# Kernel tuning notes

Measured on AMD Instinct MI355X. Metric: run time of the kernel, lower is better.

Reference implementation:

```python
import jax, jax.numpy as jnp
import numpy as np

D_MODEL = 1024
EXPAND = 2
D_INNER = D_MODEL * EXPAND  # 2048 independent SSM channels
D_STATE = 16
BATCH = 4
SEQ = 4096


def setup_inputs() -> dict:
    key = jax.random.key(0)
    ks = jax.random.split(key, 10)
    w = lambda k, shape, scale=0.02: jax.random.normal(k, shape, jnp.float32) * scale
    return {
        "x": jax.random.normal(ks[0], (BATCH, SEQ, D_MODEL), jnp.float32),
        "w_in": w(ks[1], (D_MODEL, D_INNER)),
        "b_in": jnp.zeros((D_INNER,), jnp.float32),
        "w_gate": w(ks[2], (D_MODEL, D_INNER)),
        "b_gate": jnp.zeros((D_INNER,), jnp.float32),
        # per-channel linear SSM params: h_t = A h_{t-1} + B x_t ; y_t = C . h_t
        "A": w(ks[3], (D_INNER, D_STATE, D_STATE), 0.05),  # small spectral radius -> stable recurrence
        "B_ssm": w(ks[4], (D_INNER, D_STATE), 0.1),
        "C_ssm": w(ks[5], (D_INNER, D_STATE), 0.1),
        "w_out": w(ks[6], (D_INNER, D_MODEL)),
        "b_out": jnp.zeros((D_MODEL,), jnp.float32),
    }


def reference(x, w_in, b_in, w_gate, b_gate, A, B_ssm, C_ssm, w_out, b_out):
    # x: [B, S, D]
    x_proj = x @ w_in + b_in                     # [B, S, C]
    gate = jax.nn.sigmoid(x @ w_gate + b_gate)   # [B, S, C]

    def step(h, xt):
        # h: [B, C, N] state for all channels; xt: [B, C] scalar input per channel
        h = jnp.einsum("cnm,bcm->bcn", A, h) + B_ssm[None] * xt[:, :, None]
        y = jnp.einsum("bcn,cn->bc", h, C_ssm)
        return h, y

    h0 = jnp.zeros((x.shape[0], D_INNER, D_STATE), x.dtype)
    xs = jnp.swapaxes(x_proj, 0, 1)              # [S, B, C]
    _, ys = jax.lax.scan(step, h0, xs)           # ys: [S, B, C]
    ssm_out = jnp.swapaxes(ys, 0, 1)             # [B, S, C]

    y = ssm_out * gate
    return y @ w_out + b_out                     # [B, S, D]
```

## Files before the change

kernel.cpp:

```cpp
#include <hip/hip_runtime.h>
#include <hip/hip_bf16.h>

#define D_MODEL 1024
#define D_INNER 2048
#define D_STATE 16
#define BATCH   4
#define SEQ     4096
#define MROWS   (BATCH * SEQ)

#define LTAPS 16
#define TSPAN 64

using bf16 = __hip_bfloat16;

typedef __attribute__((ext_vector_type(8))) short bf16x8;
typedef __attribute__((ext_vector_type(4))) float f32x4;

__device__ __forceinline__ float bf2f(bf16 v) { return __bfloat162float(v); }
__device__ __forceinline__ unsigned short f2bfbits(float f) {
  bf16 h = __float2bfloat16(f);
  return *(unsigned short*)&h;
}

#define AS1CAST(p) ((const __attribute__((address_space(1))) unsigned int*)(unsigned long long)(p))
#define AS3CAST(p) ((__attribute__((address_space(3))) unsigned int*)(unsigned long long)(p))

struct GemmCtx {
  const bf16* gptr[3];
  char*       lptr[3];
  int aoff[4], boff[4];
  int lane, wr, wc;
};

__device__ __forceinline__ void gemm_setup(
    GemmCtx& cx, const bf16* A, const bf16* BT, bf16* As, bf16* Bs,
    int m0, int n0, int K)
{
  const int tid  = threadIdx.x;
  cx.lane = tid & 63;
  const int wv = tid >> 6;
  cx.wr = wv >> 1;
  cx.wc = wv & 1;

  const int lrow = cx.lane >> 2;
  const int kch  = (((cx.lane & 3) ^ ((cx.lane >> 3) & 3)) * 8);
#pragma unroll
  for (int i = 0; i < 3; ++i) {
    const int s = wv * 3 + i;
    if (s < 16) {
      cx.gptr[i] = A + (size_t)(m0 + s * 16 + lrow) * K + kch;
      cx.lptr[i] = (char*)As + s * 1024;
    } else {
      const int t = s - 16;
      cx.gptr[i] = BT + (size_t)(n0 + t * 16 + lrow) * K + kch;
      cx.lptr[i] = (char*)Bs + t * 1024;
    }
  }
  const int fla = cx.lane & 15;
  const int cb  = cx.lane >> 4;
  const int csl = (cb ^ ((fla >> 1) & 3)) * 8;
#pragma unroll
  for (int i = 0; i < 4; ++i) {
    cx.aoff[i] = (cx.wr * 64 + i * 16 + fla) * 32 + csl;
    cx.boff[i] = (cx.wc * 64 + i * 16 + fla) * 32 + csl;
  }
}

__device__ __forceinline__ void gemm_kloop(
    GemmCtx& cx, const bf16* As, const bf16* Bs, f32x4 (&acc)[4][4], int K)
{
  for (int k0 = 0; k0 < K; k0 += 32) {
#pragma unroll
    for (int i = 0; i < 3; ++i)
      __builtin_amdgcn_global_load_lds(AS1CAST(cx.gptr[i]), AS3CAST(cx.lptr[i]), 16, 0, 0);
    cx.gptr[0] += 32; cx.gptr[1] += 32; cx.gptr[2] += 32;
    __syncthreads();

    bf16x8 af[4], bfr[4];
#pragma unroll
    for (int i = 0; i < 4; ++i) af[i]  = *(const bf16x8*)&As[cx.aoff[i]];
#pragma unroll
    for (int j = 0; j < 4; ++j) bfr[j] = *(const bf16x8*)&Bs[cx.boff[j]];

#pragma unroll
    for (int i = 0; i < 4; ++i)
#pragma unroll
      for (int j = 0; j < 4; ++j)
        acc[i][j] = __builtin_amdgcn_mfma_f32_16x16x32_bf16(af[i], bfr[j], acc[i][j], 0, 0, 0);
    __syncthreads();
  }
}

__global__ __launch_bounds__(512) void gemm_proj_dual(
    const bf16* __restrict__ A,
    const bf16* __restrict__ BT,
    const float* __restrict__ bias_in, const float* __restrict__ bias_gate,
    bf16* __restrict__ xp, bf16* __restrict__ gate)
{
  __shared__ alignas(16) bf16 As[256 * 32];
  __shared__ alignas(16) bf16 Bs[128 * 32];

  const int m0 = blockIdx.y * 256;
  const int n0 = blockIdx.x * 128;

  GemmCtx cx;
  gemm_setup(cx, A, BT, As, Bs, m0, n0, D_MODEL);

  f32x4 acc[4][4];
#pragma unroll
  for (int i = 0; i < 4; ++i)
#pragma unroll
    for (int j = 0; j < 4; ++j) acc[i][j] = (f32x4){0.f, 0.f, 0.f, 0.f};

  gemm_kloop(cx, As, Bs, acc, D_MODEL);

  const bool isGate = (n0 >= D_INNER);
  const int  nloc0  = n0 - (isGate ? D_INNER : 0);
  const float* bias = isGate ? bias_gate : bias_in;
  bf16* dst         = isGate ? gate : xp;

  const int crow = (cx.lane >> 4) * 4;
  const int ccol = cx.lane & 15;
#pragma unroll
  for (int i = 0; i < 4; ++i) {
#pragma unroll
    for (int j = 0; j < 4; ++j) {
      const int col = nloc0 + cx.wc * 64 + j * 16 + ccol;
      const float bcol = bias[col];
#pragma unroll
      for (int r = 0; r < 4; ++r) {
        const size_t row = (size_t)(m0 + cx.wr * 64 + i * 16 + crow + r);
        float v = acc[i][j][r] + bcol;
        if (isGate) v = 1.0f / (1.0f + __expf(-v));
        dst[row * D_INNER + col] = __float2bfloat16(v);
      }
    }
  }
}

__global__ __launch_bounds__(512) void gemm_out(
    const bf16* __restrict__ A,
    const bf16* __restrict__ BT,
    const float* __restrict__ bias,
    float* __restrict__ C)
{
  __shared__ alignas(16) bf16 As[256 * 32];
  __shared__ alignas(16) bf16 Bs[128 * 32];

  const int m0 = blockIdx.y * 256;
  const int n0 = blockIdx.x * 128;

  GemmCtx cx;
  gemm_setup(cx, A, BT, As, Bs, m0, n0, D_INNER);

  f32x4 acc[4][4];
#pragma unroll
  for (int i = 0; i < 4; ++i)
#pragma unroll
    for (int j = 0; j < 4; ++j) acc[i][j] = (f32x4){0.f, 0.f, 0.f, 0.f};

  gemm_kloop(cx, As, Bs, acc, D_INNER);

  const int crow = (cx.lane >> 4) * 4;
  const int ccol = cx.lane & 15;
#pragma unroll
  for (int i = 0; i < 4; ++i) {
#pragma unroll
    for (int j = 0; j < 4; ++j) {
      const int col = n0 + cx.wc * 64 + j * 16 + ccol;
      const float bcol = bias[col];
#pragma unroll
      for (int r = 0; r < 4; ++r) {
        const size_t row = (size_t)(m0 + cx.wr * 64 + i * 16 + crow + r);
        C[row * D_MODEL + col] = acc[i][j][r] + bcol;
      }
    }
  }
}

__global__ __launch_bounds__(256) void f32_to_bf16(
    const float* __restrict__ in, bf16* __restrict__ out, int n4)
{
  const int i = (blockIdx.x * 256 + threadIdx.x);
  if (i >= n4) return;
  const float4 v = *(const float4*)(in + (size_t)i * 4);
  ushort4 r;
  r.x = f2bfbits(v.x); r.y = f2bfbits(v.y); r.z = f2bfbits(v.z); r.w = f2bfbits(v.w);
  *(ushort4*)(out + (size_t)i * 4) = r;
}

__global__ __launch_bounds__(256) void transpose_to_bf16(
    const float* __restrict__ in, bf16* __restrict__ out, int R, int C)
{
  __shared__ float tile[32][33];
  const int c0 = blockIdx.x * 32, r0 = blockIdx.y * 32;
  const int tx = threadIdx.x & 31, ty = threadIdx.x >> 5;
#pragma unroll
  for (int i = ty; i < 32; i += 8)
    tile[i][tx] = in[(size_t)(r0 + i) * C + c0 + tx];
  __syncthreads();
#pragma unroll
  for (int i = ty; i < 32; i += 8)
    out[(size_t)(c0 + i) * R + r0 + tx] = __float2bfloat16(tile[tx][i]);
}

__device__ __forceinline__ float4 load4f(const float* p) { return *(const float4*)p; }

__global__ __launch_bounds__(256) void ssm_taps(
    const float* __restrict__ A, const float* __restrict__ Bv,
    const float* __restrict__ Cv, float* __restrict__ g)
{
  const int c = blockIdx.x * blockDim.x + threadIdx.x;
  if (c >= D_INNER) return;
  const float* Ac = A + (size_t)c * D_STATE * D_STATE;
  float v[D_STATE], cr[D_STATE];
#pragma unroll
  for (int i = 0; i < D_STATE; ++i) {
    v[i]  = Bv[(size_t)c * D_STATE + i];
    cr[i] = Cv[(size_t)c * D_STATE + i];
  }
  for (int m = 0; m < LTAPS; ++m) {
    float y = 0.f;
#pragma unroll
    for (int i = 0; i < D_STATE; ++i) y += cr[i] * v[i];
    g[(size_t)m * D_INNER + c] = y;
    float nv[D_STATE];
#pragma unroll
    for (int n = 0; n < D_STATE; ++n) {
      const float4 a0 = load4f(Ac + n * D_STATE + 0);
      const float4 a1 = load4f(Ac + n * D_STATE + 4);
      const float4 a2 = load4f(Ac + n * D_STATE + 8);
      const float4 a3 = load4f(Ac + n * D_STATE + 12);
      float s = a0.x * v[0] + a0.y * v[1] + a0.z * v[2] + a0.w * v[3];
      s += a1.x * v[4] + a1.y * v[5] + a1.z * v[6] + a1.w * v[7];
      s += a2.x * v[8] + a2.y * v[9] + a2.z * v[10] + a2.w * v[11];
      s += a3.x * v[12] + a3.y * v[13] + a3.z * v[14] + a3.w * v[15];
      nv[n] = s;
    }
#pragma unroll
    for (int i = 0; i < D_STATE; ++i) v[i] = nv[i];
  }
}

__global__ __launch_bounds__(256) void conv_gate(
    const bf16* __restrict__ xp, bf16* __restrict__ gate_io,
    const float* __restrict__ g)
{
  const int c  = blockIdx.x * blockDim.x + threadIdx.x;
  const int b  = blockIdx.z;
  const int t0 = blockIdx.y * TSPAN;

  float gg[LTAPS];
#pragma unroll
  for (int m = 0; m < LTAPS; ++m) gg[m] = g[(size_t)m * D_INNER + c];

  const size_t baseBC = ((size_t)b * SEQ) * D_INNER + c;

  float w[2 * LTAPS];
#pragma unroll
  for (int j = 0; j < LTAPS; ++j) {
    const int t = t0 - LTAPS + j;
    w[j] = (t >= 0) ? bf2f(xp[baseBC + (size_t)t * D_INNER]) : 0.f;
  }

  for (int blk = 0; blk < TSPAN; blk += LTAPS) {
#pragma unroll
    for (int j = 0; j < LTAPS; ++j)
      w[LTAPS + j] = bf2f(xp[baseBC + (size_t)(t0 + blk + j) * D_INNER]);
#pragma unroll
    for (int j = 0; j < LTAPS; ++j) {
      float y = 0.f;
#pragma unroll
      for (int m = 0; m < LTAPS; ++m) y += gg[m] * w[LTAPS + j - m];
      const size_t idx = baseBC + (size_t)(t0 + blk + j) * D_INNER;
      const float gt = bf2f(gate_io[idx]);
      gate_io[idx] = __float2bfloat16(y * gt);
    }
#pragma unroll
    for (int j = 0; j < LTAPS; ++j) w[j] = w[j + LTAPS];
  }
}

extern "C" void kernel_launch(void* const* d_in, const int* in_sizes, int n_in,
                              void* d_out, int out_size, void* d_ws, size_t ws_size,
                              hipStream_t stream)
{
  const float* x      = (const float*)d_in[0];
  const float* w_in   = (const float*)d_in[1];
  const float* b_in   = (const float*)d_in[2];
  const float* w_gate = (const float*)d_in[3];
  const float* b_gate = (const float*)d_in[4];
  const float* A      = (const float*)d_in[5];
  const float* B_ssm  = (const float*)d_in[6];
  const float* C_ssm  = (const float*)d_in[7];
  const float* w_out  = (const float*)d_in[8];
  const float* b_out  = (const float*)d_in[9];
  float* out = (float*)d_out;

  char* ws = (char*)d_ws;
  bf16*  gate  = (bf16*)(ws);
  bf16*  xbf   = (bf16*)(ws + 67108864);
  bf16*  wcatT = (bf16*)(ws + 100663296);
  bf16*  w_otT = (bf16*)(ws + 109051904);
  float* taps  = (float*)(ws + 113246208);
  bf16*  xp    = (bf16*)d_out;

  dim3 blk(256);

  hipLaunchKernelGGL(ssm_taps, dim3(D_INNER / 256), blk, 0, stream, A, B_ssm, C_ssm, taps);
  hipLaunchKernelGGL(f32_to_bf16, dim3((MROWS * D_MODEL / 4) / 256), blk, 0, stream,
                     x, xbf, MROWS * D_MODEL / 4);
  hipLaunchKernelGGL(transpose_to_bf16, dim3(D_INNER / 32, D_MODEL / 32), blk, 0, stream,
                     w_in, wcatT, D_MODEL, D_INNER);
  hipLaunchKernelGGL(transpose_to_bf16, dim3(D_INNER / 32, D_MODEL / 32), blk, 0, stream,
                     w_gate, wcatT + (size_t)D_INNER * D_MODEL, D_MODEL, D_INNER);
  hipLaunchKernelGGL(transpose_to_bf16, dim3(D_MODEL / 32, D_INNER / 32), blk, 0, stream,
                     w_out, w_otT, D_INNER, D_MODEL);

  dim3 gblk(512);
  dim3 g1(2 * D_INNER / 128, MROWS / 256);
  hipLaunchKernelGGL(gemm_proj_dual, g1, gblk, 0, stream,
                     xbf, wcatT, b_in, b_gate, xp, gate);

  dim3 gc(D_INNER / 256, SEQ / TSPAN, BATCH);
  hipLaunchKernelGGL(conv_gate, gc, blk, 0, stream, xp, gate, taps);

  dim3 g2(D_MODEL / 128, MROWS / 256);
  hipLaunchKernelGGL(gemm_out, g2, gblk, 0, stream, gate, w_otT, b_out, out);
}
```

Measured before the change: 461.4 us.

## Rewrite both GEMMs as 256x256 double-buffered pipelined kernels with block swizzle

Replaces the 256x128, K=32 single-buffered GEMM loop with a 256x256 tile, K=64 step and double-buffered LDS. Global-to-LDS loads for the next tiles are interleaved with four MFMA quadrants per step, using explicit vmcnt/lgkmcnt waits, barriers and s_setprio. Blocks are remapped through a swizzle to improve L2 reuse, and launch bounds request 2 blocks per CU. The goal is to hide memory latency and cut barrier stalls and redundant tile loads. In exchange it needs 128 KB of LDS per block and more registers, and the hand-written wait counts are fragile.

```diff
diff --git a/kernel.cpp b/kernel.cpp
--- a/kernel.cpp
+++ b/kernel.cpp
@@ -25,157 +25,256 @@
 #define AS1CAST(p) ((const __attribute__((address_space(1))) unsigned int*)(unsigned long long)(p))
 #define AS3CAST(p) ((__attribute__((address_space(3))) unsigned int*)(unsigned long long)(p))
 
-struct GemmCtx {
-  const bf16* gptr[3];
-  char*       lptr[3];
-  int aoff[4], boff[4];
-  int lane, wr, wc;
+#define FENCE() asm volatile("" ::: "memory")
+#define BAR() do { FENCE(); __builtin_amdgcn_s_barrier(); FENCE(); } while (0)
+#define WAIT_LGKM0() asm volatile("s_waitcnt lgkmcnt(0)" ::: "memory")
+
+#define TILE_E (256 * 64)
+
+struct G8 {
+  const bf16 *gA, *gB;
+  size_t K64, K128;
+  int stageLds;
+  int baseA0, baseA1;
+  int baseB0, baseB1;
+  int wr, wc, lane;
 };
 
-__device__ __forceinline__ void gemm_setup(
-    GemmCtx& cx, const bf16* A, const bf16* BT, bf16* As, bf16* Bs,
-    int m0, int n0, int K)
-{
-  const int tid  = threadIdx.x;
-  cx.lane = tid & 63;
+__device__ __forceinline__ void g8_setup(G8& g, const bf16* A, const bf16* BT,
+                                         int m0, int n0, int K)
+{
+  const int tid = threadIdx.x;
+  g.lane = tid & 63;
   const int wv = tid >> 6;
-  cx.wr = wv >> 1;
-  cx.wc = wv & 1;
-
-  const int lrow = cx.lane >> 2;
-  const int kch  = (((cx.lane & 3) ^ ((cx.lane >> 3) & 3)) * 8);
-#pragma unroll
-  for (int i = 0; i < 3; ++i) {
-    const int s = wv * 3 + i;
-    if (s < 16) {
-      cx.gptr[i] = A + (size_t)(m0 + s * 16 + lrow) * K + kch;
-      cx.lptr[i] = (char*)As + s * 1024;
-    } else {
-      const int t = s - 16;
-      cx.gptr[i] = BT + (size_t)(n0 + t * 16 + lrow) * K + kch;
-      cx.lptr[i] = (char*)Bs + t * 1024;
-    }
-  }
-  const int fla = cx.lane & 15;
-  const int cb  = cx.lane >> 4;
-  const int csl = (cb ^ ((fla >> 1) & 3)) * 8;
-#pragma unroll
-  for (int i = 0; i < 4; ++i) {
-    cx.aoff[i] = (cx.wr * 64 + i * 16 + fla) * 32 + csl;
-    cx.boff[i] = (cx.wc * 64 + i * 16 + fla) * 32 + csl;
-  }
-}
-
-__device__ __forceinline__ void gemm_kloop(
-    GemmCtx& cx, const bf16* As, const bf16* Bs, f32x4 (&acc)[4][4], int K)
-{
-  for (int k0 = 0; k0 < K; k0 += 32) {
-#pragma unroll
-    for (int i = 0; i < 3; ++i)
-      __builtin_amdgcn_global_load_lds(AS1CAST(cx.gptr[i]), AS3CAST(cx.lptr[i]), 16, 0, 0);
-    cx.gptr[0] += 32; cx.gptr[1] += 32; cx.gptr[2] += 32;
-    __syncthreads();
-
-    bf16x8 af[4], bfr[4];
-#pragma unroll
-    for (int i = 0; i < 4; ++i) af[i]  = *(const bf16x8*)&As[cx.aoff[i]];
-#pragma unroll
-    for (int j = 0; j < 4; ++j) bfr[j] = *(const bf16x8*)&Bs[cx.boff[j]];
-
-#pragma unroll
-    for (int i = 0; i < 4; ++i)
-#pragma unroll
-      for (int j = 0; j < 4; ++j)
-        acc[i][j] = __builtin_amdgcn_mfma_f32_16x16x32_bf16(af[i], bfr[j], acc[i][j], 0, 0, 0);
-    __syncthreads();
-  }
-}
-
-__global__ __launch_bounds__(512) void gemm_proj_dual(
+  g.wr = wv >> 2;
+  g.wc = wv & 3;
+  const int lr = g.lane >> 3, sl = g.lane & 7;
+  g.gA = A  + (size_t)(m0 + wv * 8 + lr) * K + (sl ^ lr) * 8;
+  g.gB = BT + (size_t)(n0 + wv * 8 + lr) * K + (sl ^ lr) * 8;
+  g.K64  = (size_t)64 * K;
+  g.K128 = (size_t)128 * K;
+  g.stageLds = wv * 8 * 64;
+  const int fla = g.lane & 15, cb = g.lane >> 4;
+  const int s0 = cb ^ (fla & 7), s1 = s0 ^ 4;
+  g.baseA0 = (g.wr * 64 + fla) * 64 + s0 * 8;
+  g.baseA1 = (g.wr * 64 + fla) * 64 + s1 * 8;
+  g.baseB0 = (g.wc * 32 + fla) * 64 + s0 * 8;
+  g.baseB1 = (g.wc * 32 + fla) * 64 + s1 * 8;
+}
+
+__device__ __forceinline__ void g8_stageA(const G8& g, bf16* dstTile, int h, int tau)
+{
+  const bf16* s = g.gA + (h ? g.K128 : (size_t)0) + (size_t)tau * 64;
+  bf16* d = dstTile + g.stageLds + h * (128 * 64);
+  __builtin_amdgcn_global_load_lds(AS1CAST(s), AS3CAST(d), 16, 0, 0);
+  __builtin_amdgcn_global_load_lds(AS1CAST(s + g.K64), AS3CAST(d + 64 * 64), 16, 0, 0);
+}
+
+__device__ __forceinline__ void g8_stageB(const G8& g, bf16* dstTile, int h, int tau)
+{
+  const bf16* s = g.gB + (h ? g.K128 : (size_t)0) + (size_t)tau * 64;
+  bf16* d = dstTile + g.stageLds + h * (128 * 64);
+  __builtin_amdgcn_global_load_lds(AS1CAST(s), AS3CAST(d), 16, 0, 0);
+  __builtin_amdgcn_global_load_lds(AS1CAST(s + g.K64), AS3CAST(d + 64 * 64), 16, 0, 0);
+}
+
+#define LOAD_A(MH) do { _Pragma("unroll") \
+  for (int mi = 0; mi < 4; ++mi) { \
+    af[mi][0] = *(const bf16x8*)&At[g.baseA0 + (MH) * 8192 + mi * 1024]; \
+    af[mi][1] = *(const bf16x8*)&At[g.baseA1 + (MH) * 8192 + mi * 1024]; \
+  } } while (0)
+
+#define LOAD_B(NH) do { _Pragma("unroll") \
+  for (int ni = 0; ni < 2; ++ni) { \
+    bfr[ni][0] = *(const bf16x8*)&Bt[g.baseB0 + (NH) * 8192 + ni * 1024]; \
+    bfr[ni][1] = *(const bf16x8*)&Bt[g.baseB1 + (NH) * 8192 + ni * 1024]; \
+  } } while (0)
+
+#define MFMA_Q(MH, NH) do { _Pragma("unroll") \
+  for (int mi = 0; mi < 4; ++mi) { _Pragma("unroll") \
+    for (int ni = 0; ni < 2; ++ni) { \
+      acc[MH][NH][mi][ni] = __builtin_amdgcn_mfma_f32_16x16x32_bf16( \
+          af[mi][0], bfr[ni][0], acc[MH][NH][mi][ni], 0, 0, 0); \
+      acc[MH][NH][mi][ni] = __builtin_amdgcn_mfma_f32_16x16x32_bf16( \
+          af[mi][1], bfr[ni][1], acc[MH][NH][mi][ni], 0, 0, 0); \
+    } } } while (0)
+
+__device__ __forceinline__ void g8_main(const G8& g, bf16* As, bf16* Bs,
+                                        f32x4 (&acc)[2][2][4][2], int K)
+{
+  const int nt = K >> 6;
+  bf16* A0 = As;  bf16* A1 = As + TILE_E;
+  bf16* B0 = Bs;  bf16* B1 = Bs + TILE_E;
+
+  g8_stageA(g, A0, 0, 0);
+  g8_stageB(g, B0, 1, 0);
+  g8_stageA(g, A0, 1, 0);
+  g8_stageB(g, B0, 0, 0);
+  if (nt > 1) {
+    g8_stageA(g, A1, 0, 1);
+    g8_stageB(g, B1, 1, 1);
+    g8_stageA(g, A1, 1, 1);
+    asm volatile("s_waitcnt vmcnt(6)" ::: "memory");
+  } else {
+    asm volatile("s_waitcnt vmcnt(0)" ::: "memory");
+  }
+  BAR();
+
+  bf16x8 af[4][2], bfr[2][2];
+
+  for (int t = 0; t < nt; ++t) {
+    const bf16* At = (t & 1) ? A1 : A0;
+    const bf16* Bt = (t & 1) ? B1 : B0;
+    bf16* Asame = (t & 1) ? A1 : A0;
+    bf16* Bsame = (t & 1) ? B1 : B0;
+    bf16* Bnext = (t & 1) ? B0 : B1;
+
+    LOAD_A(0); LOAD_B(0);
+    if (t + 1 < nt) g8_stageB(g, Bnext, 0, t + 1);
+    asm volatile("s_waitcnt lgkmcnt(8)" ::: "memory");
+    BAR();
+    WAIT_LGKM0();
+    __builtin_amdgcn_s_setprio(1);
+    MFMA_Q(0, 0);
+    __builtin_amdgcn_s_setprio(0);
+    BAR();
+
+    LOAD_B(1);
+    if (t + 2 < nt) g8_stageA(g, Asame, 0, t + 2);
+    BAR();
+    WAIT_LGKM0();
+    __builtin_amdgcn_s_setprio(1);
+    MFMA_Q(0, 1);
+    __builtin_amdgcn_s_setprio(0);
+    BAR();
+
+    LOAD_A(1);
+    if (t + 2 < nt) g8_stageB(g, Bsame, 1, t + 2);
+    BAR();
+    WAIT_LGKM0();
+    __builtin_amdgcn_s_setprio(1);
+    MFMA_Q(1, 1);
+    __builtin_amdgcn_s_setprio(0);
+    BAR();
+
+    LOAD_B(0);
+    if (t + 2 < nt) g8_stageA(g, Asame, 1, t + 2);
+    if (t < nt - 2) asm volatile("s_waitcnt vmcnt(6)" ::: "memory");
+    else            asm volatile("s_waitcnt vmcnt(0)" ::: "memory");
+    BAR();
+    WAIT_LGKM0();
+    __builtin_amdgcn_s_setprio(1);
+    MFMA_Q(1, 0);
+    __builtin_amdgcn_s_setprio(0);
+    BAR();
+  }
+}
+
+__global__ __launch_bounds__(512, 2) void gemm_proj_dual(
     const bf16* __restrict__ A,
     const bf16* __restrict__ BT,
     const float* __restrict__ bias_in, const float* __restrict__ bias_gate,
     bf16* __restrict__ xp, bf16* __restrict__ gate)
 {
-  __shared__ alignas(16) bf16 As[256 * 32];
-  __shared__ alignas(16) bf16 Bs[128 * 32];
-
-  const int m0 = blockIdx.y * 256;
-  const int n0 = blockIdx.x * 128;
-
-  GemmCtx cx;
-  gemm_setup(cx, A, BT, As, Bs, m0, n0, D_MODEL);
-
-  f32x4 acc[4][4];
-#pragma unroll
-  for (int i = 0; i < 4; ++i)
-#pragma unroll
-    for (int j = 0; j < 4; ++j) acc[i][j] = (f32x4){0.f, 0.f, 0.f, 0.f};
-
-  gemm_kloop(cx, As, Bs, acc, D_MODEL);
+  __shared__ alignas(16) bf16 As[2 * TILE_E];
+  __shared__ alignas(16) bf16 Bs[2 * TILE_E];
+
+  const int b = blockIdx.x;
+  const int swz = (b & 7) * 128 + (b >> 3);
+  const int bm = swz >> 4, bn = swz & 15;
+  const int m0 = bm * 256, n0 = bn * 256;
+
+  G8 g;
+  g8_setup(g, A, BT, m0, n0, D_MODEL);
+
+  f32x4 acc[2][2][4][2];
+#pragma unroll
+  for (int a1 = 0; a1 < 2; ++a1)
+#pragma unroll
+    for (int a2 = 0; a2 < 2; ++a2)
+#pragma unroll
+      for (int a3 = 0; a3 < 4; ++a3)
+#pragma unroll
+        for (int a4 = 0; a4 < 2; ++a4)
+          acc[a1][a2][a3][a4] = (f32x4){0.f, 0.f, 0.f, 0.f};
+
+  g8_main(g, As, Bs, acc, D_MODEL);
 
   const bool isGate = (n0 >= D_INNER);
   const int  nloc0  = n0 - (isGate ? D_INNER : 0);
   const float* bias = isGate ? bias_gate : bias_in;
   bf16* dst         = isGate ? gate : xp;
 
-  const int crow = (cx.lane >> 4) * 4;
-  const int ccol = cx.lane & 15;
-#pragma unroll
-  for (int i = 0; i < 4; ++i) {
-#pragma unroll
-    for (int j = 0; j < 4; ++j) {
-      const int col = nloc0 + cx.wc * 64 + j * 16 + ccol;
-      const float bcol = bias[col];
-#pragma unroll
-      for (int r = 0; r < 4; ++r) {
-        const size_t row = (size_t)(m0 + cx.wr * 64 + i * 16 + crow + r);
-        float v = acc[i][j][r] + bcol;
-        if (isGate) v = 1.0f / (1.0f + __expf(-v));
-        dst[row * D_INNER + col] = __float2bfloat16(v);
-      }
-    }
-  }
-}
-
-__global__ __launch_bounds__(512) void gemm_out(
+  const int crow = (g.lane >> 4) * 4;
+  const int ccol = g.lane & 15;
+#pragma unroll
+  for (int mh = 0; mh < 2; ++mh)
+#pragma unroll
+    for (int nh = 0; nh < 2; ++nh)
+#pragma unroll
+      for (int mi = 0; mi < 4; ++mi)
+#pragma unroll
+        for (int ni = 0; ni < 2; ++ni) {
+          const int col = nloc0 + nh * 128 + g.wc * 32 + ni * 16 + ccol;
+          const float bcol = bias[col];
+#pragma unroll
+          for (int r = 0; r < 4; ++r) {
+            const size_t row = (size_t)(m0 + mh * 128 + g.wr * 64 + mi * 16 + crow + r);
+            float v = acc[mh][nh][mi][ni][r] + bcol;
+            if (isGate) v = 1.0f / (1.0f + __expf(-v));
+            dst[row * D_INNER + col] = __float2bfloat16(v);
+          }
+        }
+}
+
+__global__ __launch_bounds__(512, 2) void gemm_out(
     const bf16* __restrict__ A,
     const bf16* __restrict__ BT,
     const float* __restrict__ bias,
     float* __restrict__ C)
 {
-  __shared__ alignas(16) bf16 As[256 * 32];
-  __shared__ alignas(16) bf16 Bs[128 * 32];
-
-  const int m0 = blockIdx.y * 256;
-  const int n0 = blockIdx.x * 128;
-
-  GemmCtx cx;
-  gemm_setup(cx, A, BT, As, Bs, m0, n0, D_INNER);
-
-  f32x4 acc[4][4];
-#pragma unroll
-  for (int i = 0; i < 4; ++i)
-#pragma unroll
-    for (int j = 0; j < 4; ++j) acc[i][j] = (f32x4){0.f, 0.f, 0.f, 0.f};
-
-  gemm_kloop(cx, As, Bs, acc, D_INNER);
-
-  const int crow = (cx.lane >> 4) * 4;
-  const int ccol = cx.lane & 15;
-#pragma unroll
-  for (int i = 0; i < 4; ++i) {
-#pragma unroll
-    for (int j = 0; j < 4; ++j) {
-      const int col = n0 + cx.wc * 64 + j * 16 + ccol;
-      const float bcol = bias[col];
-#pragma unroll
-      for (int r = 0; r < 4; ++r) {
-        const size_t row = (size_t)(m0 + cx.wr * 64 + i * 16 + crow + r);
-        C[row * D_MODEL + col] = acc[i][j][r] + bcol;
-      }
-    }
-  }
+  __shared__ alignas(16) bf16 As[2 * TILE_E];
+  __shared__ alignas(16) bf16 Bs[2 * TILE_E];
+
+  const int b = blockIdx.x;
+  const int swz = (b & 7) * 32 + (b >> 3);
+  const int bm = swz >> 2, bn = swz & 3;
+  const int m0 = bm * 256, n0 = bn * 256;
+
+  G8 g;
+  g8_setup(g, A, BT, m0, n0, D_INNER);
+
+  f32x4 acc[2][2][4][2];
+#pragma unroll
+  for (int a1 = 0; a1 < 2; ++a1)
+#pragma unroll
+    for (int a2 = 0; a2 < 2; ++a2)
+#pragma unroll
+      for (int a3 = 0; a3 < 4; ++a3)
+#pragma unroll
+        for (int a4 = 0; a4 < 2; ++a4)
+          acc[a1][a2][a3][a4] = (f32x4){0.f, 0.f, 0.f, 0.f};
+
+  g8_main(g, As, Bs, acc, D_INNER);
+
+  const int crow = (g.lane >> 4) * 4;
+  const int ccol = g.lane & 15;
+#pragma unroll
+  for (int mh = 0; mh < 2; ++mh)
+#pragma unroll
+    for (int nh = 0; nh < 2; ++nh)
+#pragma unroll
+      for (int mi = 0; mi < 4; ++mi)
+#pragma unroll
+        for (int ni = 0; ni < 2; ++ni) {
+          const int col = n0 + nh * 128 + g.wc * 32 + ni * 16 + ccol;
+          const float bcol = bias[col];
+#pragma unroll
+          for (int r = 0; r < 4; ++r) {
+            const size_t row = (size_t)(m0 + mh * 128 + g.wr * 64 + mi * 16 + crow + r);
+            C[row * D_MODEL + col] = acc[mh][nh][mi][ni][r] + bcol;
+          }
+        }
 }
 
 __global__ __launch_bounds__(256) void f32_to_bf16(
@@ -318,13 +417,12 @@
                      w_out, w_otT, D_INNER, D_MODEL);
 
   dim3 gblk(512);
-  dim3 g1(2 * D_INNER / 128, MROWS / 256);
-  hipLaunchKernelGGL(gemm_proj_dual, g1, gblk, 0, stream,
+  hipLaunchKernelGGL(gemm_proj_dual, dim3((2 * D_INNER / 256) * (MROWS / 256)), gblk, 0, stream,
                      xbf, wcatT, b_in, b_gate, xp, gate);
 
   dim3 gc(D_INNER / 256, SEQ / TSPAN, BATCH);
   hipLaunchKernelGGL(conv_gate, gc, blk, 0, stream, xp, gate, taps);
 
-  dim3 g2(D_MODEL / 128, MROWS / 256);
-  hipLaunchKernelGGL(gemm_out, g2, gblk, 0, stream, gate, w_otT, b_out, out);
-}
+  hipLaunchKernelGGL(gemm_out, dim3((D_MODEL / 256) * (MROWS / 256)), gblk, 0, stream,
+                     gate, w_otT, b_out, out);
+}
```

Measured after the change: 408.3 us. 1.13x faster.
